# Optimization experiments

Measured on AMD Instinct MI355X. Metric: run time of the kernel, lower is better.

Reference implementation:

```python
import jax, jax.numpy as jnp
import numpy as np

B, T, D_IN = 256, 250, 700
H1, H2, D_OUT = 256, 256, 20
B_J0 = 0.01
BETA = 1.8  # adaptation strength (isAdapt=1)
LENS, SCALE, HIGHT, GAMMA = 0.5, 6.0, 0.15, 0.5
SQRT_2PI = float(np.sqrt(2.0 * np.pi))


def _gaussian(x, mu, sigma):
    return jnp.exp(-((x - mu) ** 2) / (2.0 * sigma ** 2)) / (SQRT_2PI * sigma)


@jax.custom_vjp
def act_fun(x):
    # Heaviside spike with multi-Gaussian surrogate gradient (gradient_type='MG')
    return (x > 0).astype(x.dtype)


def _act_fwd(x):
    return act_fun(x), x


def _act_bwd(x, g):
    temp = (_gaussian(x, 0.0, LENS) * (1.0 + HIGHT)
            - _gaussian(x, LENS, SCALE * LENS) * HIGHT
            - _gaussian(x, -LENS, SCALE * LENS) * HIGHT)
    return (g * temp * GAMMA,)


act_fun.defvjp(_act_fwd, _act_bwd)


def setup_inputs() -> dict:
    key = jax.random.key(0)
    ks = jax.random.split(key, 16)
    # binary-ish spike input (SHD spike trains), rand fill
    x = (jax.random.uniform(ks[0], (B, T, D_IN)) < 0.1).astype(jnp.float32)

    def xavier(k, out_d, in_d):
        lim = float(np.sqrt(6.0 / (in_d + out_d)))
        return jax.random.uniform(k, (out_d, in_d), jnp.float32, -lim, lim)

    return {
        "x": x,
        "w_i2h1": xavier(ks[1], H1, D_IN),
        "w_h12h1": xavier(ks[2], H1, H1),
        "w_h12h2": xavier(ks[3], H2, H1),
        "w_h22h2": xavier(ks[4], H2, H2),
        "w_h2o": xavier(ks[5], D_OUT, H2),
        "b_h1": jnp.zeros((H1,), jnp.float32),
        "b_h2": jnp.zeros((H2,), jnp.float32),
        "b_o": jnp.zeros((D_OUT,), jnp.float32),
        "tau_adp_h1": 150.0 + 10.0 * jax.random.normal(ks[6], (H1,), jnp.float32),
        "tau_adp_h2": 150.0 + 10.0 * jax.random.normal(ks[7], (H2,), jnp.float32),
        "tau_m_h1": 20.0 + 5.0 * jax.random.normal(ks[8], (H1,), jnp.float32),
        "tau_m_h2": 20.0 + 5.0 * jax.random.normal(ks[9], (H2,), jnp.float32),
        "tau_m_o": 20.0 + 5.0 * jax.random.normal(ks[10], (D_OUT,), jnp.float32),
    }


def _lif_step(inp, mem, spk, b, alpha, ro):
    # mem_update_adp with params=None, dparams=None, isAdapt=1, dt=1, R_m=1
    b = ro * b + BETA * (1.0 - ro) * spk
    mem = mem * alpha - b * spk + (1.0 - alpha) * inp
    spk = act_fun(mem - b - B_J0)
    return mem, spk, b


def reference(x, w_i2h1, w_h12h1, w_h12h2, w_h22h2, w_h2o,
              b_h1, b_h2, b_o, tau_adp_h1, tau_adp_h2,
              tau_m_h1, tau_m_h2, tau_m_o):
    bsz = x.shape[0]
    h1, h2, d_out = w_i2h1.shape[0], w_h12h2.shape[0], w_h2o.shape[0]

    alpha1 = jnp.exp(-1.0 / tau_m_h1)
    ro1 = jnp.exp(-1.0 / tau_adp_h1)
    alpha2 = jnp.exp(-1.0 / tau_m_h2)
    ro2 = jnp.exp(-1.0 / tau_adp_h2)
    alpha_o = jnp.exp(-1.0 / tau_m_o)

    init = (
        jnp.zeros((bsz, h1)), jnp.zeros((bsz, h1)), jnp.full((bsz, h1), B_J0),
        jnp.zeros((bsz, h2)), jnp.zeros((bsz, h2)), jnp.full((bsz, h2), B_J0),
        jnp.zeros((bsz, d_out)), jnp.zeros((bsz, d_out)),
    )
    xT = jnp.swapaxes(x, 0, 1)  # [T, B, D_in]

    def step(carry, xt):
        mem1, spk1, bb1, mem2, spk2, bb2, mem_o, acc = carry
        h1_in = xt @ w_i2h1.T + spk1 @ w_h12h1.T + b_h1
        mem1, spk1, bb1 = _lif_step(h1_in, mem1, spk1, bb1, alpha1, ro1)
        h2_in = spk1 @ w_h12h2.T + spk2 @ w_h22h2.T + b_h2
        mem2, spk2, bb2 = _lif_step(h2_in, mem2, spk2, bb2, alpha2, ro2)
        o_in = spk2 @ w_h2o.T + b_o
        mem_o = mem_o * alpha_o + (1.0 - alpha_o) * o_in  # output_Neuron
        acc = acc + jax.nn.softmax(mem_o, axis=-1)
        return (mem1, spk1, bb1, mem2, spk2, bb2, mem_o, acc), None

    carry, _ = jax.lax.scan(step, init, xT)
    return carry[-1]  # accumulated softmax over the 250 timesteps, [B, 20]
```

## Files before the change

### kernel.cpp

```cpp
#include <hip/hip_runtime.h>
#include <cstdint>
#include <cstddef>

#define BB 256
#define TT 250
#define DIN 700
#define H1 256
#define H2 256
#define DOUT 20
#define BJ0 0.01f
#define BETAC 1.8f
#define DUMMY 256
#define IQSCALE 3.814697265625e-06f

typedef float f32x4 __attribute__((ext_vector_type(4)));
typedef short s16x4 __attribute__((ext_vector_type(4)));

#define IOFF_P12 89728
#define SOFF_T22 311040
#define FOFF_W2O 188416
#define FOFF_XP  193556
#define FOFF_MO  16577556
#define N_TRANS  316180

#define BARRIER_LDS() asm volatile("s_waitcnt lgkmcnt(0)\n\ts_barrier" ::: "memory")

__device__ __forceinline__ short q18(float w) {
    float s = w * 262144.0f;
    s = fminf(fmaxf(s, -32767.0f), 32767.0f);
    return (short)__float2int_rn(s);
}

__global__ void transpose_all_k(const float* __restrict__ w_i2h1,
                                const float* __restrict__ w_h12h1,
                                const float* __restrict__ w_h12h2,
                                const float* __restrict__ w_h22h2,
                                const float* __restrict__ w_h2o,
                                short* __restrict__ sws,
                                float* __restrict__ fws) {
    int i = blockIdx.x * blockDim.x + threadIdx.x;
    if (i < 179456) { int d = i >> 8, h = i & 255;
        sws[i] = q18((d < DIN) ? w_i2h1[h * DIN + d] : 0.f); return; }
    i -= 179456;
    if (i < 65792) { int d = i >> 8, h = i & 255;
        unsigned int lo = 0, hi = 0;
        if (d < H1) {
            lo = (unsigned short)q18(w_h12h1[h * H1 + d]);
            hi = (unsigned short)q18(w_h12h2[h * H1 + d]);
        }
        ((int*)sws)[IOFF_P12 + i] = (int)(lo | (hi << 16)); return; }
    i -= 65792;
    if (i < 65792) { int d = i >> 8, h = i & 255;
        sws[SOFF_T22 + i] = q18((d < H2) ? w_h22h2[h * H2 + d] : 0.f); return; }
    i -= 65792;
    if (i < 5140)  { int j = i / 20, h = i % 20;
        fws[FOFF_W2O + i] = (j < H2) ? w_h2o[h * H2 + j] : 0.f; return; }
}

__global__ __launch_bounds__(256) void xproj_k(const float* __restrict__ x,
                                               const short* __restrict__ sT1,
                                               const float* __restrict__ b_h1,
                                               float* __restrict__ Xp) {
    const int lane = threadIdx.x & 63;
    const int wv   = threadIdx.x >> 6;
    const int bt   = blockIdx.x * 4 + wv;
    const int b    = bt / TT;
    const int t    = bt - b * TT;

    __shared__ __align__(16) int lst[4][712];

    const float* xrow = x + ((size_t)b * TT + t) * DIN;
    float xv[11];
    #pragma unroll
    for (int c = 0; c < 11; ++c) {
        int d = c * 64 + lane;
        xv[c] = (d < DIN) ? __builtin_nontemporal_load(xrow + d) : 0.f;
    }
    int cnt = 0;
    #pragma unroll
    for (int c = 0; c < 11; ++c) {
        int d = c * 64 + lane;
        bool p = (xv[c] != 0.0f);
        unsigned long long m = __ballot(p ? 1 : 0);
        if (p) {
            int pos = cnt + __popcll(m & ((1ull << lane) - 1ull));
            lst[wv][pos] = d;
        }
        cnt += __popcll(m);
    }
    int cntp = (cnt + 15) & ~15;
    if (lane < cntp - cnt) lst[wv][cnt + lane] = DIN;
    __syncthreads();

    const int lo = lane * 4;
    int i0 = 0, i1 = 0, i2 = 0, i3 = 0;
    int j0 = 0, j1 = 0, j2 = 0, j3 = 0;
    for (int k = 0; k < cntp; k += 16) {
        int4 ja = *(const int4*)&lst[wv][k];
        int4 jb = *(const int4*)&lst[wv][k + 4];
        int4 jc = *(const int4*)&lst[wv][k + 8];
        int4 jd = *(const int4*)&lst[wv][k + 12];
        s16x4 w0  = *(const s16x4*)(sT1 + ((size_t)ja.x << 8) + lo);
        s16x4 w1  = *(const s16x4*)(sT1 + ((size_t)ja.y << 8) + lo);
        s16x4 w2  = *(const s16x4*)(sT1 + ((size_t)ja.z << 8) + lo);
        s16x4 w3  = *(const s16x4*)(sT1 + ((size_t)ja.w << 8) + lo);
        s16x4 w4  = *(const s16x4*)(sT1 + ((size_t)jb.x << 8) + lo);
        s16x4 w5  = *(const s16x4*)(sT1 + ((size_t)jb.y << 8) + lo);
        s16x4 w6  = *(const s16x4*)(sT1 + ((size_t)jb.z << 8) + lo);
        s16x4 w7  = *(const s16x4*)(sT1 + ((size_t)jb.w << 8) + lo);
        s16x4 w8  = *(const s16x4*)(sT1 + ((size_t)jc.x << 8) + lo);
        s16x4 w9  = *(const s16x4*)(sT1 + ((size_t)jc.y << 8) + lo);
        s16x4 w10 = *(const s16x4*)(sT1 + ((size_t)jc.z << 8) + lo);
        s16x4 w11 = *(const s16x4*)(sT1 + ((size_t)jc.w << 8) + lo);
        s16x4 w12 = *(const s16x4*)(sT1 + ((size_t)jd.x << 8) + lo);
        s16x4 w13 = *(const s16x4*)(sT1 + ((size_t)jd.y << 8) + lo);
        s16x4 w14 = *(const s16x4*)(sT1 + ((size_t)jd.z << 8) + lo);
        s16x4 w15 = *(const s16x4*)(sT1 + ((size_t)jd.w << 8) + lo);
        i0 += ((w0.x + w1.x) + (w2.x + w3.x)) + ((w4.x + w5.x) + (w6.x + w7.x));
        i1 += ((w0.y + w1.y) + (w2.y + w3.y)) + ((w4.y + w5.y) + (w6.y + w7.y));
        i2 += ((w0.z + w1.z) + (w2.z + w3.z)) + ((w4.z + w5.z) + (w6.z + w7.z));
        i3 += ((w0.w + w1.w) + (w2.w + w3.w)) + ((w4.w + w5.w) + (w6.w + w7.w));
        j0 += ((w8.x + w9.x) + (w10.x + w11.x)) + ((w12.x + w13.x) + (w14.x + w15.x));
        j1 += ((w8.y + w9.y) + (w10.y + w11.y)) + ((w12.y + w13.y) + (w14.y + w15.y));
        j2 += ((w8.z + w9.z) + (w10.z + w11.z)) + ((w12.z + w13.z) + (w14.z + w15.z));
        j3 += ((w8.w + w9.w) + (w10.w + w11.w)) + ((w12.w + w13.w) + (w14.w + w15.w));
    }
    f32x4 acc = *(const f32x4*)(b_h1 + lo);
    acc.x += (float)(i0 + j0) * IQSCALE;
    acc.y += (float)(i1 + j1) * IQSCALE;
    acc.z += (float)(i2 + j2) * IQSCALE;
    acc.w += (float)(i3 + j3) * IQSCALE;
    __builtin_nontemporal_store(acc, (f32x4*)(Xp + ((size_t)b * TT + t) * H1 + lo));
}

__global__ __launch_bounds__(512) void rec_k(
    const float* __restrict__ Xp,
    const int*   __restrict__ sP12,
    const short* __restrict__ sT22, const float* __restrict__ wT2o,
    const float* __restrict__ b_h2, const float* __restrict__ b_o,
    const float* __restrict__ tau_adp_h1, const float* __restrict__ tau_adp_h2,
    const float* __restrict__ tau_m_h1, const float* __restrict__ tau_m_h2,
    const float* __restrict__ tau_m_o,
    float* __restrict__ Mo) {
    const int tid  = threadIdx.x;
    const int h    = tid & 255;
    const int half = tid >> 8;
    const int lane = tid & 63;
    const int g    = tid >> 6;
    const int l4   = lane << 2;
    const int b    = blockIdx.x;
    const float* __restrict__ XpB = Xp + (size_t)b * TT * H1;
    float* __restrict__ MoB = Mo + (size_t)b * TT * DOUT;

    __shared__ __align__(16) short sT22L[65792];
    __shared__ __align__(16) int lst1s[2][256];
    __shared__ __align__(16) int lst2s[2][256];
    __shared__ __align__(16) int lcnt[2][2];
    __shared__ __align__(16) int pp11[8][256];
    __shared__ __align__(16) int pp12[8][256];
    __shared__ __align__(16) int pp22[8][256];
    __shared__ __align__(16) float pro[8][20];

    {
        const int* src = (const int*)sT22;
        int* dst = (int*)sT22L;
        for (int i2 = tid; i2 < 32896; i2 += 512) dst[i2] = src[i2];
        if (tid < 4) lcnt[tid >> 1][tid & 1] = 0;
    }

    const float alpha1 = expf(-1.0f / tau_m_h1[h]);
    const float ro1    = expf(-1.0f / tau_adp_h1[h]);
    const float alpha2 = expf(-1.0f / tau_m_h2[h]);
    const float ro2    = expf(-1.0f / tau_adp_h2[h]);
    const float bh2v   = b_h2[h];
    float alpo = 0.f, bov = 0.f;
    if (h < DOUT) { alpo = expf(-1.0f / tau_m_o[h]); bov = b_o[h]; }

    float mem1 = 0.f, spk1 = 0.f, bb1v = BJ0;
    float mem2 = 0.f, spk2 = 0.f, bb2v = BJ0;
    float memo = 0.f;

    float xp_cur = 0.f;
    if (half == 0) xp_cur = __builtin_nontemporal_load(XpB + h);
    __syncthreads();

    for (int i = 0; i <= TT + 1; ++i) {
        const int cur = i & 1, nxt = cur ^ 1;

        float xp_nxt = 0.f;
        if (half == 0 && i + 1 < TT)
            xp_nxt = __builtin_nontemporal_load(XpB + (size_t)(i + 1) * H1 + h);

        const int tot1 = lcnt[cur][0];
        const int tot2 = lcnt[cur][1];
        const int n1p = (tot1 + 31) & ~31;
        const int n2p = (tot2 + 31) & ~31;

        if (half == 0) lst1s[nxt][h] = DUMMY; else lst2s[nxt][h] = DUMMY;
        if (tid == 0)   lcnt[nxt][0] = 0;
        if (tid == 256) lcnt[nxt][1] = 0;

        int a110 = 0, a111 = 0, a112 = 0, a113 = 0;
        int a120 = 0, a121 = 0, a122 = 0, a123 = 0;
        int a220 = 0, a221 = 0, a222 = 0, a223 = 0;
        float ao0 = 0.f, ao1 = 0.f, ao2 = 0.f, ao3 = 0.f;

        const int gbase = g << 5;
        const int ng1 = n1p >> 3;
        for (int kk = 0; kk < ng1; kk += 4) {
            int4 e = *(const int4*)&lst1s[cur][gbase + kk];
            int4 pa = *(const int4*)(sP12 + ((size_t)e.x << 8) + l4);
            int4 pb = *(const int4*)(sP12 + ((size_t)e.y << 8) + l4);
            int4 pc = *(const int4*)(sP12 + ((size_t)e.z << 8) + l4);
            int4 pd = *(const int4*)(sP12 + ((size_t)e.w << 8) + l4);
            a110 += ((int)(short)pa.x + (int)(short)pb.x) + ((int)(short)pc.x + (int)(short)pd.x);
            a111 += ((int)(short)pa.y + (int)(short)pb.y) + ((int)(short)pc.y + (int)(short)pd.y);
            a112 += ((int)(short)pa.z + (int)(short)pb.z) + ((int)(short)pc.z + (int)(short)pd.z);
            a113 += ((int)(short)pa.w + (int)(short)pb.w) + ((int)(short)pc.w + (int)(short)pd.w);
            a120 += ((pa.x >> 16) + (pb.x >> 16)) + ((pc.x >> 16) + (pd.x >> 16));
            a121 += ((pa.y >> 16) + (pb.y >> 16)) + ((pc.y >> 16) + (pd.y >> 16));
            a122 += ((pa.z >> 16) + (pb.z >> 16)) + ((pc.z >> 16) + (pd.z >> 16));
            a123 += ((pa.w >> 16) + (pb.w >> 16)) + ((pc.w >> 16) + (pd.w >> 16));
        }
        const int ng2 = n2p >> 3;
        for (int kk = 0; kk < ng2; kk += 4) {
            int4 e = *(const int4*)&lst2s[cur][gbase + kk];
            s16x4 wa = *(const s16x4*)(sT22L + (e.x << 8) + l4);
            s16x4 wb = *(const s16x4*)(sT22L + (e.y << 8) + l4);
            s16x4 wc = *(const s16x4*)(sT22L + (e.z << 8) + l4);
            s16x4 wd = *(const s16x4*)(sT22L + (e.w << 8) + l4);
            a220 += (wa.x + wb.x) + (wc.x + wd.x);
            a221 += (wa.y + wb.y) + (wc.y + wd.y);
            a222 += (wa.z + wb.z) + (wc.z + wd.z);
            a223 += (wa.w + wb.w) + (wc.w + wd.w);
            if (lane < 5) {
                float4 va = *(const float4*)(wT2o + e.x * DOUT + l4);
                float4 vb = *(const float4*)(wT2o + e.y * DOUT + l4);
                float4 vc = *(const float4*)(wT2o + e.z * DOUT + l4);
                float4 vd = *(const float4*)(wT2o + e.w * DOUT + l4);
                ao0 += (va.x + vb.x) + (vc.x + vd.x);
                ao1 += (va.y + vb.y) + (vc.y + vd.y);
                ao2 += (va.z + vb.z) + (vc.z + vd.z);
                ao3 += (va.w + vb.w) + (vc.w + vd.w);
            }
        }
        {
            int4 v;
            v.x = a110; v.y = a111; v.z = a112; v.w = a113;
            *(int4*)&pp11[g][l4] = v;
            v.x = a120; v.y = a121; v.z = a122; v.w = a123;
            *(int4*)&pp12[g][l4] = v;
            v.x = a220; v.y = a221; v.z = a222; v.w = a223;
            *(int4*)&pp22[g][l4] = v;
        }
        if (lane < 5) {
            float4 v; v.x = ao0; v.y = ao1; v.z = ao2; v.w = ao3;
            *(float4*)&pro[g][l4] = v;
        }
        BARRIER_LDS();

        if (half == 0) {
            if (i < TT) {
                int ir11 = ((pp11[0][h] + pp11[1][h]) + (pp11[2][h] + pp11[3][h]))
                         + ((pp11[4][h] + pp11[5][h]) + (pp11[6][h] + pp11[7][h]));
                float r1 = (float)ir11 * IQSCALE;
                bb1v = ro1 * bb1v + BETAC * (1.f - ro1) * spk1;
                mem1 = mem1 * alpha1 - bb1v * spk1 + (1.f - alpha1) * (xp_cur + r1);
                float ns1 = (mem1 - bb1v - BJ0) > 0.f ? 1.f : 0.f;
                spk1 = ns1;
                unsigned long long m1 = __ballot(ns1 != 0.f ? 1 : 0);
                int c = __popcll(m1);
                int base = 0;
                if (lane == 0) base = atomicAdd(&lcnt[nxt][0], c);
                base = __shfl(base, 0);
                if (ns1 != 0.f) {
                    int pos = base + __popcll(m1 & ((1ull << lane) - 1ull));
                    lst1s[nxt][((pos & 7) << 5) + (pos >> 3)] = h;
                }
            }
        } else {
            if (i >= 1 && i <= TT) {
                int ir12 = ((pp12[0][h] + pp12[1][h]) + (pp12[2][h] + pp12[3][h]))
                         + ((pp12[4][h] + pp12[5][h]) + (pp12[6][h] + pp12[7][h]));
                int ir22 = ((pp22[0][h] + pp22[1][h]) + (pp22[2][h] + pp22[3][h]))
                         + ((pp22[4][h] + pp22[5][h]) + (pp22[6][h] + pp22[7][h]));
                float r23 = (float)(ir22 + ir12) * IQSCALE;
                bb2v = ro2 * bb2v + BETAC * (1.f - ro2) * spk2;
                mem2 = mem2 * alpha2 - bb2v * spk2 + (1.f - alpha2) * (bh2v + r23);
                float ns2 = (mem2 - bb2v - BJ0) > 0.f ? 1.f : 0.f;
                spk2 = ns2;
                unsigned long long m2 = __ballot(ns2 != 0.f ? 1 : 0);
                int c = __popcll(m2);
                int base = 0;
                if (lane == 0) base = atomicAdd(&lcnt[nxt][1], c);
                base = __shfl(base, 0);
                if (ns2 != 0.f) {
                    int pos = base + __popcll(m2 & ((1ull << lane) - 1ull));
                    lst2s[nxt][((pos & 7) << 5) + (pos >> 3)] = h;
                }
            }
            if ((h < DOUT) && (i >= 2)) {
                float ro = ((pro[0][h] + pro[1][h]) + (pro[2][h] + pro[3][h]))
                         + ((pro[4][h] + pro[5][h]) + (pro[6][h] + pro[7][h]));
                memo = memo * alpo + (1.f - alpo) * (bov + ro);
                __builtin_nontemporal_store(memo, MoB + (size_t)(i - 2) * DOUT + h);
            }
        }
        BARRIER_LDS();

        xp_cur = xp_nxt;
    }
}

__global__ __launch_bounds__(256) void soft_k(const float* __restrict__ Mo,
                                              float* __restrict__ out) {
    const int b = blockIdx.x;
    const int t = threadIdx.x;
    __shared__ float sm[TT][DOUT];

    if (t < TT) {
        const float* row = Mo + ((size_t)b * TT + t) * DOUT;
        float v[DOUT];
        #pragma unroll
        for (int k = 0; k < DOUT; k += 4) {
            float4 r = *(const float4*)(row + k);
            v[k] = r.x; v[k + 1] = r.y; v[k + 2] = r.z; v[k + 3] = r.w;
        }
        float mx = v[0];
        #pragma unroll
        for (int j = 1; j < DOUT; ++j) mx = fmaxf(mx, v[j]);
        float s = 0.f;
        #pragma unroll
        for (int j = 0; j < DOUT; ++j) { v[j] = __expf(v[j] - mx); s += v[j]; }
        float inv = 1.0f / s;
        #pragma unroll
        for (int j = 0; j < DOUT; ++j) sm[t][j] = v[j] * inv;
    }
    __syncthreads();
    if (t < DOUT) {
        float acc = 0.f;
        for (int tt = 0; tt < TT; ++tt) acc += sm[tt][t];
        out[b * DOUT + t] = acc;
    }
}

extern "C" void kernel_launch(void* const* d_in, const int* in_sizes, int n_in,
                              void* d_out, int out_size, void* d_ws, size_t ws_size,
                              hipStream_t stream) {
    const float* x          = (const float*)d_in[0];
    const float* w_i2h1     = (const float*)d_in[1];
    const float* w_h12h1    = (const float*)d_in[2];
    const float* w_h12h2    = (const float*)d_in[3];
    const float* w_h22h2    = (const float*)d_in[4];
    const float* w_h2o      = (const float*)d_in[5];
    const float* b_h1       = (const float*)d_in[6];
    const float* b_h2       = (const float*)d_in[7];
    const float* b_o        = (const float*)d_in[8];
    const float* tau_adp_h1 = (const float*)d_in[9];
    const float* tau_adp_h2 = (const float*)d_in[10];
    const float* tau_m_h1   = (const float*)d_in[11];
    const float* tau_m_h2   = (const float*)d_in[12];
    const float* tau_m_o    = (const float*)d_in[13];

    short* sws = (short*)d_ws;
    float* fws = (float*)d_ws;
    const short* sT1  = sws;
    const int*   sP12 = (const int*)d_ws + IOFF_P12;
    const short* sT22 = sws + SOFF_T22;
    float* wT2o = fws + FOFF_W2O;
    float* Xp   = fws + FOFF_XP;
    float* Mo   = fws + FOFF_MO;

    transpose_all_k<<<(N_TRANS + 255) / 256, 256, 0, stream>>>(
        w_i2h1, w_h12h1, w_h12h2, w_h22h2, w_h2o, sws, fws);

    xproj_k<<<(BB * TT) / 4, 256, 0, stream>>>(x, sT1, b_h1, Xp);

    rec_k<<<BB, 512, 0, stream>>>(Xp, sP12, sT22, wT2o,
                                  b_h2, b_o, tau_adp_h1, tau_adp_h2,
                                  tau_m_h1, tau_m_h2, tau_m_o, Mo);

    soft_k<<<BB, 256, 0, stream>>>(Mo, (float*)d_out);
}
```

Before: 797.8 us.

## Replace sparse gather input projection with int8 MFMA GEMM using split weights

The input projection no longer gathers weight rows for nonzero spike indices per timestep. It now runs a dense int8 MFMA GEMM: spikes are packed as 0/1 bytes and the 16-bit quantized weights are split into high and low int8 halves, which are recombined as (hi<<8)+lo. The goal is to move the projection from scattered memory accesses onto matrix cores with LDS tiling. In exchange it does dense work over all 700 inputs even though only about 10% are active, and it adds a second GEMM pass for the low byte.

```diff
diff --git a/kernel.cpp b/kernel.cpp
--- a/kernel.cpp
+++ b/kernel.cpp
@@ -15,13 +15,15 @@
 
 typedef float f32x4 __attribute__((ext_vector_type(4)));
 typedef short s16x4 __attribute__((ext_vector_type(4)));
-
-#define IOFF_P12 89728
-#define SOFF_T22 311040
-#define FOFF_W2O 188416
-#define FOFF_XP  193556
-#define FOFF_MO  16577556
-#define N_TRANS  316180
+typedef int   i32x4 __attribute__((ext_vector_type(4)));
+
+#define COFF_BL  180224
+#define IOFF_P12 90112
+#define SOFF_T22 311808
+#define FOFF_W2O 188800
+#define FOFF_XP  193944
+#define FOFF_MO  16577944
+#define N_TRANS  316948
 
 #define BARRIER_LDS() asm volatile("s_waitcnt lgkmcnt(0)\n\ts_barrier" ::: "memory")
 
@@ -36,19 +38,29 @@
                                 const float* __restrict__ w_h12h2,
                                 const float* __restrict__ w_h22h2,
                                 const float* __restrict__ w_h2o,
+                                signed char* __restrict__ cws,
                                 short* __restrict__ sws,
+                                int* __restrict__ iws,
                                 float* __restrict__ fws) {
     int i = blockIdx.x * blockDim.x + threadIdx.x;
-    if (i < 179456) { int d = i >> 8, h = i & 255;
-        sws[i] = q18((d < DIN) ? w_i2h1[h * DIN + d] : 0.f); return; }
-    i -= 179456;
+    if (i < 180224) {
+        int h = i / 704, k = i - h * 704;
+        int q = (k < DIN) ? (int)q18(w_i2h1[h * DIN + k]) : 0;
+        q = q > 32639 ? 32639 : (q < -32640 ? -32640 : q);
+        int hi = (q + 128) >> 8;
+        int lo = q - (hi << 8);
+        cws[i] = (signed char)hi;
+        cws[COFF_BL + i] = (signed char)lo;
+        return;
+    }
+    i -= 180224;
     if (i < 65792) { int d = i >> 8, h = i & 255;
         unsigned int lo = 0, hi = 0;
         if (d < H1) {
             lo = (unsigned short)q18(w_h12h1[h * H1 + d]);
             hi = (unsigned short)q18(w_h12h2[h * H1 + d]);
         }
-        ((int*)sws)[IOFF_P12 + i] = (int)(lo | (hi << 16)); return; }
+        iws[IOFF_P12 + i] = (int)(lo | (hi << 16)); return; }
     i -= 65792;
     if (i < 65792) { int d = i >> 8, h = i & 255;
         sws[SOFF_T22 + i] = q18((d < H2) ? w_h22h2[h * H2 + d] : 0.f); return; }
@@ -57,80 +69,93 @@
         fws[FOFF_W2O + i] = (j < H2) ? w_h2o[h * H2 + j] : 0.f; return; }
 }
 
-__global__ __launch_bounds__(256) void xproj_k(const float* __restrict__ x,
-                                               const short* __restrict__ sT1,
+__global__ __launch_bounds__(256) void xgemm_k(const float* __restrict__ x,
+                                               const signed char* __restrict__ Bh,
+                                               const signed char* __restrict__ Bl,
                                                const float* __restrict__ b_h1,
                                                float* __restrict__ Xp) {
-    const int lane = threadIdx.x & 63;
-    const int wv   = threadIdx.x >> 6;
-    const int bt   = blockIdx.x * 4 + wv;
-    const int b    = bt / TT;
-    const int t    = bt - b * TT;
-
-    __shared__ __align__(16) int lst[4][712];
-
-    const float* xrow = x + ((size_t)b * TT + t) * DIN;
-    float xv[11];
+    const int t    = threadIdx.x;
+    const int lane = t & 63;
+    const int w    = t >> 6;
+    const int m0   = blockIdx.x * 32;
+
+    __shared__ __align__(16) signed char Asub[32 * 720];
+    __shared__ __align__(16) signed char Bhs[256 * 80];
+    __shared__ __align__(16) signed char Bls[256 * 80];
+
     #pragma unroll
-    for (int c = 0; c < 11; ++c) {
-        int d = c * 64 + lane;
-        xv[c] = (d < DIN) ? __builtin_nontemporal_load(xrow + d) : 0.f;
-    }
-    int cnt = 0;
+    for (int it = 0; it < 22; ++it) {
+        int flat = it * 256 + t;
+        int row  = flat / 176;
+        int c4   = flat - row * 176;
+        unsigned int pk = 0u;
+        if (c4 < 175) {
+            const float* xr = x + (size_t)(m0 + row) * DIN;
+            float4 f = *(const float4*)(xr + (c4 << 2));
+            pk = (f.x != 0.f ? 1u : 0u)
+               | (f.y != 0.f ? 1u : 0u) << 8
+               | (f.z != 0.f ? 1u : 0u) << 16
+               | (f.w != 0.f ? 1u : 0u) << 24;
+        }
+        *(unsigned int*)(Asub + row * 720 + (c4 << 2)) = pk;
+    }
+
+    i32x4 acch[2][4], accl[2][4];
     #pragma unroll
-    for (int c = 0; c < 11; ++c) {
-        int d = c * 64 + lane;
-        bool p = (xv[c] != 0.0f);
-        unsigned long long m = __ballot(p ? 1 : 0);
-        if (p) {
-            int pos = cnt + __popcll(m & ((1ull << lane) - 1ull));
-            lst[wv][pos] = d;
-        }
-        cnt += __popcll(m);
-    }
-    int cntp = (cnt + 15) & ~15;
-    if (lane < cntp - cnt) lst[wv][cnt + lane] = DIN;
-    __syncthreads();
-
-    const int lo = lane * 4;
-    int i0 = 0, i1 = 0, i2 = 0, i3 = 0;
-    int j0 = 0, j1 = 0, j2 = 0, j3 = 0;
-    for (int k = 0; k < cntp; k += 16) {
-        int4 ja = *(const int4*)&lst[wv][k];
-        int4 jb = *(const int4*)&lst[wv][k + 4];
-        int4 jc = *(const int4*)&lst[wv][k + 8];
-        int4 jd = *(const int4*)&lst[wv][k + 12];
-        s16x4 w0  = *(const s16x4*)(sT1 + ((size_t)ja.x << 8) + lo);
-        s16x4 w1  = *(const s16x4*)(sT1 + ((size_t)ja.y << 8) + lo);
-        s16x4 w2  = *(const s16x4*)(sT1 + ((size_t)ja.z << 8) + lo);
-        s16x4 w3  = *(const s16x4*)(sT1 + ((size_t)ja.w << 8) + lo);
-        s16x4 w4  = *(const s16x4*)(sT1 + ((size_t)jb.x << 8) + lo);
-        s16x4 w5  = *(const s16x4*)(sT1 + ((size_t)jb.y << 8) + lo);
-        s16x4 w6  = *(const s16x4*)(sT1 + ((size_t)jb.z << 8) + lo);
-        s16x4 w7  = *(const s16x4*)(sT1 + ((size_t)jb.w << 8) + lo);
-        s16x4 w8  = *(const s16x4*)(sT1 + ((size_t)jc.x << 8) + lo);
-        s16x4 w9  = *(const s16x4*)(sT1 + ((size_t)jc.y << 8) + lo);
-        s16x4 w10 = *(const s16x4*)(sT1 + ((size_t)jc.z << 8) + lo);
-        s16x4 w11 = *(const s16x4*)(sT1 + ((size_t)jc.w << 8) + lo);
-        s16x4 w12 = *(const s16x4*)(sT1 + ((size_t)jd.x << 8) + lo);
-        s16x4 w13 = *(const s16x4*)(sT1 + ((size_t)jd.y << 8) + lo);
-        s16x4 w14 = *(const s16x4*)(sT1 + ((size_t)jd.z << 8) + lo);
-        s16x4 w15 = *(const s16x4*)(sT1 + ((size_t)jd.w << 8) + lo);
-        i0 += ((w0.x + w1.x) + (w2.x + w3.x)) + ((w4.x + w5.x) + (w6.x + w7.x));
-        i1 += ((w0.y + w1.y) + (w2.y + w3.y)) + ((w4.y + w5.y) + (w6.y + w7.y));
-        i2 += ((w0.z + w1.z) + (w2.z + w3.z)) + ((w4.z + w5.z) + (w6.z + w7.z));
-        i3 += ((w0.w + w1.w) + (w2.w + w3.w)) + ((w4.w + w5.w) + (w6.w + w7.w));
-        j0 += ((w8.x + w9.x) + (w10.x + w11.x)) + ((w12.x + w13.x) + (w14.x + w15.x));
-        j1 += ((w8.y + w9.y) + (w10.y + w11.y)) + ((w12.y + w13.y) + (w14.y + w15.y));
-        j2 += ((w8.z + w9.z) + (w10.z + w11.z)) + ((w12.z + w13.z) + (w14.z + w15.z));
-        j3 += ((w8.w + w9.w) + (w10.w + w11.w)) + ((w12.w + w13.w) + (w14.w + w15.w));
-    }
-    f32x4 acc = *(const f32x4*)(b_h1 + lo);
-    acc.x += (float)(i0 + j0) * IQSCALE;
-    acc.y += (float)(i1 + j1) * IQSCALE;
-    acc.z += (float)(i2 + j2) * IQSCALE;
-    acc.w += (float)(i3 + j3) * IQSCALE;
-    __builtin_nontemporal_store(acc, (f32x4*)(Xp + ((size_t)b * TT + t) * H1 + lo));
+    for (int mt = 0; mt < 2; ++mt)
+        #pragma unroll
+        for (int nt = 0; nt < 4; ++nt) {
+            acch[mt][nt] = (i32x4){0, 0, 0, 0};
+            accl[mt][nt] = (i32x4){0, 0, 0, 0};
+        }
+
+    const int arow  = lane & 15;
+    const int kg16  = (lane >> 4) << 4;
+    const int bcol0 = w << 6;
+
+    for (int ks = 0; ks < 11; ++ks) {
+        __syncthreads();
+        #pragma unroll
+        for (int it2 = 0; it2 < 4; ++it2) {
+            int row = it2 * 64 + (t >> 2);
+            int ch  = (t & 3) << 4;
+            int go  = row * 704 + ks * 64 + ch;
+            *(int4*)(Bhs + row * 80 + ch) = *(const int4*)(Bh + go);
+            *(int4*)(Bls + row * 80 + ch) = *(const int4*)(Bl + go);
+        }
+        __syncthreads();
+
+        const int ko = ks * 64 + kg16;
+        i32x4 a0 = *(const i32x4*)(Asub + arow * 720 + ko);
+        i32x4 a1 = *(const i32x4*)(Asub + (16 + arow) * 720 + ko);
+        #pragma unroll
+        for (int nt = 0; nt < 4; ++nt) {
+            const int bb = (bcol0 + nt * 16 + arow) * 80 + kg16;
+            i32x4 bhf = *(const i32x4*)(Bhs + bb);
+            i32x4 blf = *(const i32x4*)(Bls + bb);
+            acch[0][nt] = __builtin_amdgcn_mfma_i32_16x16x64_i8(a0, bhf, acch[0][nt], 0, 0, 0);
+            acch[1][nt] = __builtin_amdgcn_mfma_i32_16x16x64_i8(a1, bhf, acch[1][nt], 0, 0, 0);
+            accl[0][nt] = __builtin_amdgcn_mfma_i32_16x16x64_i8(a0, blf, accl[0][nt], 0, 0, 0);
+            accl[1][nt] = __builtin_amdgcn_mfma_i32_16x16x64_i8(a1, blf, accl[1][nt], 0, 0, 0);
+        }
+    }
+
+    const int crb = (lane >> 4) << 2;
+    #pragma unroll
+    for (int nt = 0; nt < 4; ++nt) {
+        int col = bcol0 + nt * 16 + arow;
+        float bias = b_h1[col];
+        #pragma unroll
+        for (int mt = 0; mt < 2; ++mt) {
+            #pragma unroll
+            for (int r = 0; r < 4; ++r) {
+                int row = m0 + mt * 16 + crb + r;
+                int ir = (acch[mt][nt][r] << 8) + accl[mt][nt][r];
+                __builtin_nontemporal_store(bias + (float)ir * IQSCALE,
+                                            Xp + (size_t)row * H1 + col);
+            }
+        }
+    }
 }
 
 __global__ __launch_bounds__(512) void rec_k(
@@ -362,19 +387,22 @@
     const float* tau_m_h2   = (const float*)d_in[12];
     const float* tau_m_o    = (const float*)d_in[13];
 
+    signed char* cws = (signed char*)d_ws;
     short* sws = (short*)d_ws;
+    int*   iws = (int*)d_ws;
     float* fws = (float*)d_ws;
-    const short* sT1  = sws;
-    const int*   sP12 = (const int*)d_ws + IOFF_P12;
+    const signed char* Bh = cws;
+    const signed char* Bl = cws + COFF_BL;
+    const int*   sP12 = iws + IOFF_P12;
     const short* sT22 = sws + SOFF_T22;
     float* wT2o = fws + FOFF_W2O;
     float* Xp   = fws + FOFF_XP;
     float* Mo   = fws + FOFF_MO;
 
     transpose_all_k<<<(N_TRANS + 255) / 256, 256, 0, stream>>>(
-        w_i2h1, w_h12h1, w_h12h2, w_h22h2, w_h2o, sws, fws);
-
-    xproj_k<<<(BB * TT) / 4, 256, 0, stream>>>(x, sT1, b_h1, Xp);
+        w_i2h1, w_h12h1, w_h12h2, w_h22h2, w_h2o, cws, sws, iws, fws);
+
+    xgemm_k<<<(BB * TT) / 32, 256, 0, stream>>>(x, Bh, Bl, b_h1, Xp);
 
     rec_k<<<BB, 512, 0, stream>>>(Xp, sP12, sT22, wT2o,
                                   b_h2, b_o, tau_adp_h1, tau_adp_h2,
```

Result: faster. 753.8 us (-5.5%).
